# Optimization experiments

Measured on AMD Instinct MI355X. Metric: run time of the kernel, lower is better.

Reference implementation:

```python
import jax, jax.numpy as jnp
import numpy as np

EMBED_DIM = 32  # module-level constant used for the 1/sqrt(d) scale in the source
DROP_P = 0.2


def setup_inputs() -> dict:
    key = jax.random.key(0)
    kx, kq, kk, kv = jax.random.split(key, 4)
    B, T, C = 8, 4096, EMBED_DIM
    x = jax.random.normal(kx, (B, T, C), dtype=jnp.float32)
    Wq = jax.random.normal(kq, (C, C), dtype=jnp.float32) * (1.0 / np.sqrt(C))
    Wk = jax.random.normal(kk, (C, C), dtype=jnp.float32) * (1.0 / np.sqrt(C))
    Wv = jax.random.normal(kv, (C, C), dtype=jnp.float32) * (1.0 / np.sqrt(C))
    return {"x": x, "Wq": Wq, "Wk": Wk, "Wv": Wv}


def reference(x, Wq, Wk, Wv):
    B, T, C = x.shape
    # bias-free linear projections: y = x @ W.T (torch nn.Linear convention)
    q = jnp.einsum('btc,dc->btd', x, Wq)
    k = jnp.einsum('btc,dc->btd', x, Wk)
    v = jnp.einsum('btc,dc->btd', x, Wv)
    # scaled scores [B, T, T]
    att = jnp.einsum('btd,bsd->bts', q, k) / jnp.sqrt(jnp.float32(EMBED_DIM))
    causal = jnp.tril(jnp.ones((T, T), dtype=bool))
    att = jnp.where(causal, att, -jnp.inf)
    wei = jax.nn.softmax(att, axis=-1)
    # dropout on attention weights (training mode, p=0.2), deterministic key
    keep = jax.random.bernoulli(jax.random.key(42), 1.0 - DROP_P, wei.shape)
    wei = jnp.where(keep, wei / (1.0 - DROP_P), 0.0)
    return jnp.einsum('bts,bsd->btd', wei, v)
```

## Files before the change

kernel.cpp:

```cpp
#include <hip/hip_runtime.h>
#include <stdint.h>

#define BB 8
#define TTN 4096
#define CCH 32
#define WIN 128
#define KEEP_LT9 3435974144u

typedef __attribute__((ext_vector_type(8))) short bf16x8;
typedef __attribute__((ext_vector_type(4))) float f32x4;

union B8 { uint32_t u[4]; uint4 q; bf16x8 v; };

__device__ __forceinline__ uint32_t cvt_pk_bf16(float lo, float hi) {
    uint32_t d;
    asm("v_cvt_pk_bf16_f32 %0, %1, %2" : "=v"(d) : "v"(lo), "v"(hi));
    return d;
}

__device__ __forceinline__ uint32_t rotl32(uint32_t x, int r) {
    return __builtin_amdgcn_alignbit(x, x, 32 - r);
}

__device__ __forceinline__ uint32_t mask_bits(uint32_t idx) {
    uint32_t x0 = 0u, x1 = idx + 42u;
    const uint32_t K2 = 42u ^ 0x1BD11BDAu;
#define TFR(r) { x0 += x1; x1 = rotl32(x1, (r)); x1 ^= x0; }
    TFR(13) TFR(15) TFR(26) TFR(6)
    x0 += 42u; x1 += K2 + 1u;
    TFR(17) TFR(29) TFR(16) TFR(24)
    x0 += K2; x1 += 2u;
    TFR(13) TFR(15) TFR(26) TFR(6)
    x1 += 42u + 3u;
    TFR(17) TFR(29) TFR(16) TFR(24)
    x0 += 42u; x1 += K2 + 4u;
    TFR(13) TFR(15) TFR(26) TFR(6)
    x0 += K2; x1 += 5u;
#undef TFR
    return x0 ^ x1;
}

__device__ __forceinline__ void threefry4(uint32_t i0, uint32_t i1, uint32_t i2, uint32_t i3,
                                          uint32_t& o0, uint32_t& o1, uint32_t& o2, uint32_t& o3) {
    const uint32_t K2 = 42u ^ 0x1BD11BDAu;
    uint32_t a0 = 0u, a1 = 0u, a2 = 0u, a3 = 0u;
    uint32_t b0 = i0 + 42u, b1 = i1 + 42u, b2 = i2 + 42u, b3 = i3 + 42u;
#define R4(r)                                                                  \
    { a0 += b0; a1 += b1; a2 += b2; a3 += b3;                                  \
      b0 = rotl32(b0, (r)); b1 = rotl32(b1, (r));                              \
      b2 = rotl32(b2, (r)); b3 = rotl32(b3, (r));                              \
      b0 ^= a0; b1 ^= a1; b2 ^= a2; b3 ^= a3; }
#define INJ(da, db)                                                            \
    { a0 += (da); a1 += (da); a2 += (da); a3 += (da);                          \
      b0 += (db); b1 += (db); b2 += (db); b3 += (db); }
    R4(13) R4(15) R4(26) R4(6)
    INJ(42u, K2 + 1u)
    R4(17) R4(29) R4(16) R4(24)
    INJ(K2, 2u)
    R4(13) R4(15) R4(26) R4(6)
    INJ(0u, 42u + 3u)
    R4(17) R4(29) R4(16) R4(24)
    INJ(42u, K2 + 4u)
    R4(13) R4(15) R4(26) R4(6)
    INJ(K2, 5u)
#undef R4
#undef INJ
    o0 = a0 ^ b0; o1 = a1 ^ b1; o2 = a2 ^ b2; o3 = a3 ^ b3;
}

__global__ __launch_bounds__(256) void proj_qkv(const float* __restrict__ x,
                                                const float* __restrict__ Wq,
                                                const float* __restrict__ Wk,
                                                const float* __restrict__ Wv,
                                                float* __restrict__ Qf,
                                                uint16_t* __restrict__ Kb,
                                                uint16_t* __restrict__ Vt) {
    __shared__ float sW[3][CCH * CCH];
    __shared__ uint16_t vs[256][34];
    const int tid = threadIdx.x;
    for (int i = tid; i < CCH * CCH; i += 256) {
        sW[0][i] = Wq[i]; sW[1][i] = Wk[i]; sW[2][i] = Wv[i];
    }
    __syncthreads();
    const int row = blockIdx.x * 256 + tid;
    const float4* xp = reinterpret_cast<const float4*>(x + (size_t)row * CCH);
    float xr[CCH];
    #pragma unroll
    for (int i = 0; i < 8; ++i) {
        float4 t4 = xp[i];
        xr[4*i] = t4.x; xr[4*i+1] = t4.y; xr[4*i+2] = t4.z; xr[4*i+3] = t4.w;
    }
    const float scale = 0.17677669529663687f;
    #pragma unroll
    for (int mtx = 0; mtx < 3; ++mtx) {
        float o[CCH];
        #pragma unroll
        for (int d = 0; d < CCH; ++d) {
            float s0 = 0.f, s1 = 0.f, s2 = 0.f, s3 = 0.f;
            #pragma unroll
            for (int c = 0; c < CCH; c += 4) {
                s0 += xr[c]   * sW[mtx][d*CCH + c];
                s1 += xr[c+1] * sW[mtx][d*CCH + c+1];
                s2 += xr[c+2] * sW[mtx][d*CCH + c+2];
                s3 += xr[c+3] * sW[mtx][d*CCH + c+3];
            }
            o[d] = (s0 + s1) + (s2 + s3);
            if (mtx == 0) o[d] *= scale;
        }
        if (mtx == 0) {
            float4* op = reinterpret_cast<float4*>(Qf + (size_t)row * CCH);
            #pragma unroll
            for (int i = 0; i < 8; ++i)
                op[i] = make_float4(o[4*i], o[4*i+1], o[4*i+2], o[4*i+3]);
        } else if (mtx == 1) {
            uint32_t dw[16];
            #pragma unroll
            for (int k = 0; k < 16; ++k) dw[k] = cvt_pk_bf16(o[2*k], o[2*k+1]);
            uint4* kp = reinterpret_cast<uint4*>((char*)Kb + (size_t)row * 64);
            #pragma unroll
            for (int q = 0; q < 4; ++q)
                kp[q] = make_uint4(dw[4*q], dw[4*q+1], dw[4*q+2], dw[4*q+3]);
        } else {
            #pragma unroll
            for (int k = 0; k < 16; ++k)
                *reinterpret_cast<uint32_t*>(&vs[tid][2*k]) = cvt_pk_bf16(o[2*k], o[2*k+1]);
        }
    }
    __syncthreads();
    const int b = blockIdx.x >> 4, seg = blockIdx.x & 15;
    const int d = tid >> 3, part = tid & 7;
    uint32_t dw[16];
    #pragma unroll
    for (int k = 0; k < 16; ++k) {
        const uint32_t lo = vs[part*32 + 2*k][d];
        const uint32_t hi = vs[part*32 + 2*k + 1][d];
        dw[k] = lo | (hi << 16);
    }
    uint16_t* dst = Vt + (size_t)b * (CCH * TTN) + (size_t)d * TTN + seg * 256 + part * 32;
    uint4* dp = reinterpret_cast<uint4*>(dst);
    #pragma unroll
    for (int q = 0; q < 4; ++q)
        dp[q] = make_uint4(dw[4*q], dw[4*q+1], dw[4*q+2], dw[4*q+3]);
}

__global__ __launch_bounds__(512, 4) void attn_mfma(const float* __restrict__ Qf,
                                                    const uint16_t* __restrict__ Kb,
                                                    const uint16_t* __restrict__ Vt,
                                                    float* __restrict__ out) {
    __shared__ __align__(16) char smem[9728];

    const int j = blockIdx.x;
    const int b = j & 7;
    const int u = j >> 3;
    const int tile = (u < 32) ? (127 - u) : (u < 64) ? (u - 32)
                   : (u < 96) ? (159 - u) : (u - 64);

    const int w = threadIdx.x >> 6;
    const int lane = threadIdx.x & 63;
    const int tl = lane & 15;
    const int g = lane >> 4;
    const int thalf = w & 1;
    const int sg = w >> 1;
    const int slb = sg * 32;
    const int t0 = tile * 32;
    const int t_g = t0 + thalf * 16 + tl;

    const float* qrow = Qf + ((size_t)b * TTN + t_g) * CCH + g * 8;
    const float4 qa = *reinterpret_cast<const float4*>(qrow);
    const float4 qb = *reinterpret_cast<const float4*>(qrow + 4);
    B8 qf;
    qf.u[0] = cvt_pk_bf16(qa.x, qa.y); qf.u[1] = cvt_pk_bf16(qa.z, qa.w);
    qf.u[2] = cvt_pk_bf16(qb.x, qb.y); qf.u[3] = cvt_pk_bf16(qb.z, qb.w);

    f32x4 acc0 = {0.f,0.f,0.f,0.f}, acc1 = {0.f,0.f,0.f,0.f};
    float m = -1e30f, l = 0.f;

    const char* Kbb = (const char*)Kb + (size_t)b * TTN * 64;
    const char* Vbb = (const char*)Vt + (size_t)b * CCH * TTN * 2;
    const uint32_t idxb = ((uint32_t)b << 24) | ((uint32_t)t_g << 12);

    const int nwin = (32 * tile + 159) >> 7;

#define ATT_WINDOW(S0, TAIL)                                                   \
    {                                                                          \
        const int srow = (S0) + slb;                                           \
        B8 ka, kc, va, vc, pf;                                                 \
        ka.q = *reinterpret_cast<const uint4*>(Kbb + (size_t)(srow + tl) * 64 + g * 16); \
        kc.q = *reinterpret_cast<const uint4*>(Kbb + (size_t)(srow + 16 + tl) * 64 + g * 16); \
        va.q = *reinterpret_cast<const uint4*>(Vbb + (size_t)tl * 8192 + (size_t)(srow + g * 8) * 2); \
        vc.q = *reinterpret_cast<const uint4*>(Vbb + (size_t)(16 + tl) * 8192 + (size_t)(srow + g * 8) * 2); \
              \
        const uint32_t ib = idxb | (uint32_t)(srow + 4 * g);                   \
        uint32_t r0, r1, r2, r3, r4, r5, r6, r7;                               \
        threefry4(ib,       ib + 1u,  ib + 2u,  ib + 3u,  r0, r1, r2, r3);     \
        threefry4(ib + 16u, ib + 17u, ib + 18u, ib + 19u, r4, r5, r6, r7);     \
        const float f0 = (r0 < KEEP_LT9) ? 1.f : 0.f;                          \
        const float f1 = (r1 < KEEP_LT9) ? 1.f : 0.f;                          \
        const float f2 = (r2 < KEEP_LT9) ? 1.f : 0.f;                          \
        const float f3 = (r3 < KEEP_LT9) ? 1.f : 0.f;                          \
        const float f4 = (r4 < KEEP_LT9) ? 1.f : 0.f;                          \
        const float f5 = (r5 < KEEP_LT9) ? 1.f : 0.f;                          \
        const float f6 = (r6 < KEEP_LT9) ? 1.f : 0.f;                          \
        const float f7 = (r7 < KEEP_LT9) ? 1.f : 0.f;                          \
        const f32x4 zz = {0.f,0.f,0.f,0.f};                                    \
        f32x4 d0 = __builtin_amdgcn_mfma_f32_16x16x32_bf16(ka.v, qf.v, zz, 0, 0, 0); \
        f32x4 d1 = __builtin_amdgcn_mfma_f32_16x16x32_bf16(kc.v, qf.v, zz, 0, 0, 0); \
        if (TAIL) {                                                            \
            const int sv = srow + 4 * g;                                       \
            d0.x = (sv + 0  <= t_g) ? d0.x : -1e30f;                           \
            d0.y = (sv + 1  <= t_g) ? d0.y : -1e30f;                           \
            d0.z = (sv + 2  <= t_g) ? d0.z : -1e30f;                           \
            d0.w = (sv + 3  <= t_g) ? d0.w : -1e30f;                           \
            d1.x = (sv + 16 <= t_g) ? d1.x : -1e30f;                           \
            d1.y = (sv + 17 <= t_g) ? d1.y : -1e30f;                           \
            d1.z = (sv + 18 <= t_g) ? d1.z : -1e30f;                           \
            d1.w = (sv + 19 <= t_g) ? d1.w : -1e30f;                           \
        }                                                                      \
        float mx = fmaxf(fmaxf(fmaxf(d0.x, d0.y), fmaxf(d0.z, d0.w)),          \
                         fmaxf(fmaxf(d1.x, d1.y), fmaxf(d1.z, d1.w)));         \
        mx = fmaxf(mx, __shfl_xor(mx, 16));                                    \
        mx = fmaxf(mx, __shfl_xor(mx, 32));                                    \
        const bool up = mx > m + 8.0f;               \
        const float corr = up ? __expf(m - mx) : 1.0f;                         \
        m = up ? mx : m;                                                       \
        l *= corr; acc0 *= corr; acc1 *= corr;                                 \
        float p0 = __expf(d0.x - m), p1 = __expf(d0.y - m);                    \
        float p2 = __expf(d0.z - m), p3 = __expf(d0.w - m);                    \
        float p4 = __expf(d1.x - m), p5 = __expf(d1.y - m);                    \
        float p6 = __expf(d1.z - m), p7 = __expf(d1.w - m);                    \
        if (TAIL) {                                                            \
            const float alive = (srow <= t_g) ? 1.0f : 0.0f;                   \
            p0 *= alive; p1 *= alive; p2 *= alive; p3 *= alive;                \
            p4 *= alive; p5 *= alive; p6 *= alive; p7 *= alive;                \
        }                                                                      \
        float ls = ((p0 + p1) + (p2 + p3)) + ((p4 + p5) + (p6 + p7));          \
        ls += __shfl_xor(ls, 16);                                              \
        ls += __shfl_xor(ls, 32);                                              \
        l += ls;                                                               \
        const uint32_t k00 = cvt_pk_bf16(p0 * f0, p1 * f1);                    \
        const uint32_t k01 = cvt_pk_bf16(p2 * f2, p3 * f3);                    \
        const uint32_t k10 = cvt_pk_bf16(p4 * f4, p5 * f5);                    \
        const uint32_t k11 = cvt_pk_bf16(p6 * f6, p7 * f7);                    \
        const int srcA = 16 * ((g & 1) * 2) + tl;                              \
        const int srcB = srcA + 16;                                            \
        const uint32_t a0 = (uint32_t)__shfl((int)k00, srcA);                  \
        const uint32_t b0 = (uint32_t)__shfl((int)k10, srcA);                  \
        const uint32_t a1 = (uint32_t)__shfl((int)k01, srcA);                  \
        const uint32_t b1 = (uint32_t)__shfl((int)k11, srcA);                  \
        const uint32_t a2 = (uint32_t)__shfl((int)k00, srcB);                  \
        const uint32_t b2 = (uint32_t)__shfl((int)k10, srcB);                  \
        const uint32_t a3 = (uint32_t)__shfl((int)k01, srcB);                  \
        const uint32_t b3 = (uint32_t)__shfl((int)k11, srcB);                  \
        const bool hi = (g >= 2);                                              \
        pf.u[0] = hi ? b0 : a0; pf.u[1] = hi ? b1 : a1;                        \
        pf.u[2] = hi ? b2 : a2; pf.u[3] = hi ? b3 : a3;                        \
        acc0 = __builtin_amdgcn_mfma_f32_16x16x32_bf16(va.v, pf.v, acc0, 0, 0, 0); \
        acc1 = __builtin_amdgcn_mfma_f32_16x16x32_bf16(vc.v, pf.v, acc1, 0, 0, 0); \
    }

    #pragma unroll 1
    for (int win = 0; win < nwin - 1; ++win) {
        ATT_WINDOW(win << 7, 0)
    }
    {
        const int s0 = (nwin - 1) << 7;
        if (s0 + slb <= t0 + thalf * 16 + 15) ATT_WINDOW(s0, 1)
    }
#undef ATT_WINDOW

#define SLOT(TH, S) reinterpret_cast<float*>(smem + ((TH) * 2 + (S)) * 2432)
#define PUBLISH(SB)                                                            \
    {                                                                          \
        float* sb = (SB);                                                      \
        *reinterpret_cast<float4*>(sb + tl * 36 + 4 * g)      = make_float4(acc0.x, acc0.y, acc0.z, acc0.w); \
        *reinterpret_cast<float4*>(sb + tl * 36 + 16 + 4 * g) = make_float4(acc1.x, acc1.y, acc1.z, acc1.w); \
        if (g == 0) { sb[576 + 2 * tl] = m; sb[577 + 2 * tl] = l; }            \
    }
#define CONSUME(SB)                                                            \
    {                                                                          \
        const float* sb = (SB);                                                \
        const float m2 = sb[576 + 2 * tl], l2 = sb[577 + 2 * tl];              \
        const float4 x0 = *reinterpret_cast<const float4*>(sb + tl * 36 + 4 * g); \
        const float4 x1 = *reinterpret_cast<const float4*>(sb + tl * 36 + 16 + 4 * g); \
        const float mn = fmaxf(m, m2);                                         \
        const float ca = __expf(m - mn), cb = __expf(m2 - mn);                 \
        l = l * ca + l2 * cb;                                                  \
        acc0.x = acc0.x * ca + x0.x * cb; acc0.y = acc0.y * ca + x0.y * cb;    \
        acc0.z = acc0.z * ca + x0.z * cb; acc0.w = acc0.w * ca + x0.w * cb;    \
        acc1.x = acc1.x * ca + x1.x * cb; acc1.y = acc1.y * ca + x1.y * cb;    \
        acc1.z = acc1.z * ca + x1.z * cb; acc1.w = acc1.w * ca + x1.w * cb;    \
        m = mn;                                                                \
    }
    if (sg >= 2) PUBLISH(SLOT(thalf, sg - 2))
    __syncthreads();
    if (sg < 2) CONSUME(SLOT(thalf, sg))
    __syncthreads();
    if (sg == 1) PUBLISH(SLOT(thalf, 0))
    __syncthreads();
    if (sg == 0) {
        CONSUME(SLOT(thalf, 0))
        const float inv = 1.0f / (0.8f * l);
        float* orow = out + ((size_t)b * TTN + t_g) * CCH;
        *reinterpret_cast<float4*>(orow + 4 * g) =
            make_float4(acc0.x * inv, acc0.y * inv, acc0.z * inv, acc0.w * inv);
        *reinterpret_cast<float4*>(orow + 16 + 4 * g) =
            make_float4(acc1.x * inv, acc1.y * inv, acc1.z * inv, acc1.w * inv);
    }
#undef SLOT
#undef PUBLISH
#undef CONSUME
}

extern "C" void kernel_launch(void* const* d_in, const int* in_sizes, int n_in,
                              void* d_out, int out_size, void* d_ws, size_t ws_size,
                              hipStream_t stream) {
    const float* x  = (const float*)d_in[0];
    const float* Wq = (const float*)d_in[1];
    const float* Wk = (const float*)d_in[2];
    const float* Wv = (const float*)d_in[3];
    float* outp = (float*)d_out;

    float*    Qf = (float*)d_ws;
    uint16_t* Kb = (uint16_t*)((char*)d_ws + 4194304);
    uint16_t* Vt = (uint16_t*)((char*)d_ws + 6291456);

    proj_qkv<<<(BB * TTN) / 256, 256, 0, stream>>>(x, Wq, Wk, Wv, Qf, Kb, Vt);
    attn_mfma<<<1024, 512, 0, stream>>>(Qf, Kb, Vt, outp);
}
```

Baseline: 168.2 us.

## Split attention blocks into 16-row halves with 256 threads and longest-first ordering

Each attention block now handles one 16-query half-tile with 4 waves instead of both halves with 8 waves, doubling the grid to 2048 blocks of 256 threads. Tiles are issued in strictly descending causal length instead of the previous interleaved order, and the loop count is computed per half so the shorter half skips unneeded windows. The dropout mask is also applied as a select on the probability rather than a multiply by a 0/1 factor. The intent is finer-grained load balancing and less wasted work on causal tails, at the cost of loading K/V separately for each half.

```diff
diff --git a/kernel.cpp b/kernel.cpp
--- a/kernel.cpp
+++ b/kernel.cpp
@@ -20,24 +20,6 @@
 
 __device__ __forceinline__ uint32_t rotl32(uint32_t x, int r) {
     return __builtin_amdgcn_alignbit(x, x, 32 - r);
-}
-
-__device__ __forceinline__ uint32_t mask_bits(uint32_t idx) {
-    uint32_t x0 = 0u, x1 = idx + 42u;
-    const uint32_t K2 = 42u ^ 0x1BD11BDAu;
-#define TFR(r) { x0 += x1; x1 = rotl32(x1, (r)); x1 ^= x0; }
-    TFR(13) TFR(15) TFR(26) TFR(6)
-    x0 += 42u; x1 += K2 + 1u;
-    TFR(17) TFR(29) TFR(16) TFR(24)
-    x0 += K2; x1 += 2u;
-    TFR(13) TFR(15) TFR(26) TFR(6)
-    x1 += 42u + 3u;
-    TFR(17) TFR(29) TFR(16) TFR(24)
-    x0 += 42u; x1 += K2 + 4u;
-    TFR(13) TFR(15) TFR(26) TFR(6)
-    x0 += K2; x1 += 5u;
-#undef TFR
-    return x0 ^ x1;
 }
 
 __device__ __forceinline__ void threefry4(uint32_t i0, uint32_t i1, uint32_t i2, uint32_t i3,
@@ -143,27 +125,25 @@
         dp[q] = make_uint4(dw[4*q], dw[4*q+1], dw[4*q+2], dw[4*q+3]);
 }
 
-__global__ __launch_bounds__(512, 4) void attn_mfma(const float* __restrict__ Qf,
+__global__ __launch_bounds__(256, 8) void attn_mfma(const float* __restrict__ Qf,
                                                     const uint16_t* __restrict__ Kb,
                                                     const uint16_t* __restrict__ Vt,
                                                     float* __restrict__ out) {
-    __shared__ __align__(16) char smem[9728];
+    __shared__ __align__(16) char smem[4864];
 
     const int j = blockIdx.x;
     const int b = j & 7;
-    const int u = j >> 3;
-    const int tile = (u < 32) ? (127 - u) : (u < 64) ? (u - 32)
-                   : (u < 96) ? (159 - u) : (u - 64);
+    const int thalf = (j >> 3) & 1;
+    const int tile = 127 - (j >> 4);
 
     const int w = threadIdx.x >> 6;
     const int lane = threadIdx.x & 63;
     const int tl = lane & 15;
     const int g = lane >> 4;
-    const int thalf = w & 1;
-    const int sg = w >> 1;
+    const int sg = w;
     const int slb = sg * 32;
-    const int t0 = tile * 32;
-    const int t_g = t0 + thalf * 16 + tl;
+    const int tbase = tile * 32 + thalf * 16;
+    const int t_g = tbase + tl;
 
     const float* qrow = Qf + ((size_t)b * TTN + t_g) * CCH + g * 8;
     const float4 qa = *reinterpret_cast<const float4*>(qrow);
@@ -179,7 +159,7 @@
     const char* Vbb = (const char*)Vt + (size_t)b * CCH * TTN * 2;
     const uint32_t idxb = ((uint32_t)b << 24) | ((uint32_t)t_g << 12);
 
-    const int nwin = (32 * tile + 159) >> 7;
+    const int nwin = ((tbase + 15) >> 7) + 1;
 
 #define ATT_WINDOW(S0, TAIL)                                                   \
     {                                                                          \
@@ -189,19 +169,11 @@
         kc.q = *reinterpret_cast<const uint4*>(Kbb + (size_t)(srow + 16 + tl) * 64 + g * 16); \
         va.q = *reinterpret_cast<const uint4*>(Vbb + (size_t)tl * 8192 + (size_t)(srow + g * 8) * 2); \
         vc.q = *reinterpret_cast<const uint4*>(Vbb + (size_t)(16 + tl) * 8192 + (size_t)(srow + g * 8) * 2); \
-              \
+               \
         const uint32_t ib = idxb | (uint32_t)(srow + 4 * g);                   \
         uint32_t r0, r1, r2, r3, r4, r5, r6, r7;                               \
         threefry4(ib,       ib + 1u,  ib + 2u,  ib + 3u,  r0, r1, r2, r3);     \
         threefry4(ib + 16u, ib + 17u, ib + 18u, ib + 19u, r4, r5, r6, r7);     \
-        const float f0 = (r0 < KEEP_LT9) ? 1.f : 0.f;                          \
-        const float f1 = (r1 < KEEP_LT9) ? 1.f : 0.f;                          \
-        const float f2 = (r2 < KEEP_LT9) ? 1.f : 0.f;                          \
-        const float f3 = (r3 < KEEP_LT9) ? 1.f : 0.f;                          \
-        const float f4 = (r4 < KEEP_LT9) ? 1.f : 0.f;                          \
-        const float f5 = (r5 < KEEP_LT9) ? 1.f : 0.f;                          \
-        const float f6 = (r6 < KEEP_LT9) ? 1.f : 0.f;                          \
-        const float f7 = (r7 < KEEP_LT9) ? 1.f : 0.f;                          \
         const f32x4 zz = {0.f,0.f,0.f,0.f};                                    \
         f32x4 d0 = __builtin_amdgcn_mfma_f32_16x16x32_bf16(ka.v, qf.v, zz, 0, 0, 0); \
         f32x4 d1 = __builtin_amdgcn_mfma_f32_16x16x32_bf16(kc.v, qf.v, zz, 0, 0, 0); \
@@ -237,10 +209,16 @@
         ls += __shfl_xor(ls, 16);                                              \
         ls += __shfl_xor(ls, 32);                                              \
         l += ls;                                                               \
-        const uint32_t k00 = cvt_pk_bf16(p0 * f0, p1 * f1);                    \
-        const uint32_t k01 = cvt_pk_bf16(p2 * f2, p3 * f3);                    \
-        const uint32_t k10 = cvt_pk_bf16(p4 * f4, p5 * f5);                    \
-        const uint32_t k11 = cvt_pk_bf16(p6 * f6, p7 * f7);                    \
+        const float q0 = (r0 < KEEP_LT9) ? p0 : 0.f;        \
+        const float q1 = (r1 < KEEP_LT9) ? p1 : 0.f;                           \
+        const float q2 = (r2 < KEEP_LT9) ? p2 : 0.f;                           \
+        const float q3 = (r3 < KEEP_LT9) ? p3 : 0.f;                           \
+        const float q4 = (r4 < KEEP_LT9) ? p4 : 0.f;                           \
+        const float q5 = (r5 < KEEP_LT9) ? p5 : 0.f;                           \
+        const float q6 = (r6 < KEEP_LT9) ? p6 : 0.f;                           \
+        const float q7 = (r7 < KEEP_LT9) ? p7 : 0.f;                           \
+        const uint32_t k00 = cvt_pk_bf16(q0, q1), k01 = cvt_pk_bf16(q2, q3);   \
+        const uint32_t k10 = cvt_pk_bf16(q4, q5), k11 = cvt_pk_bf16(q6, q7);   \
         const int srcA = 16 * ((g & 1) * 2) + tl;                              \
         const int srcB = srcA + 16;                                            \
         const uint32_t a0 = (uint32_t)__shfl((int)k00, srcA);                  \
@@ -264,11 +242,11 @@
     }
     {
         const int s0 = (nwin - 1) << 7;
-        if (s0 + slb <= t0 + thalf * 16 + 15) ATT_WINDOW(s0, 1)
+        if (s0 + slb <= tbase + 15) ATT_WINDOW(s0, 1)
     }
 #undef ATT_WINDOW
 
-#define SLOT(TH, S) reinterpret_cast<float*>(smem + ((TH) * 2 + (S)) * 2432)
+#define SLOT(S) reinterpret_cast<float*>(smem + (S) * 2432)
 #define PUBLISH(SB)                                                            \
     {                                                                          \
         float* sb = (SB);                                                      \
@@ -291,14 +269,14 @@
         acc1.z = acc1.z * ca + x1.z * cb; acc1.w = acc1.w * ca + x1.w * cb;    \
         m = mn;                                                                \
     }
-    if (sg >= 2) PUBLISH(SLOT(thalf, sg - 2))
-    __syncthreads();
-    if (sg < 2) CONSUME(SLOT(thalf, sg))
-    __syncthreads();
-    if (sg == 1) PUBLISH(SLOT(thalf, 0))
+    if (sg >= 2) PUBLISH(SLOT(sg - 2))
+    __syncthreads();
+    if (sg < 2) CONSUME(SLOT(sg))
+    __syncthreads();
+    if (sg == 1) PUBLISH(SLOT(0))
     __syncthreads();
     if (sg == 0) {
-        CONSUME(SLOT(thalf, 0))
+        CONSUME(SLOT(0))
         const float inv = 1.0f / (0.8f * l);
         float* orow = out + ((size_t)b * TTN + t_g) * CCH;
         *reinterpret_cast<float4*>(orow + 4 * g) =
@@ -325,5 +303,5 @@
     uint16_t* Vt = (uint16_t*)((char*)d_ws + 6291456);
 
     proj_qkv<<<(BB * TTN) / 256, 256, 0, stream>>>(x, Wq, Wk, Wv, Qf, Kb, Vt);
-    attn_mfma<<<1024, 512, 0, stream>>>(Qf, Kb, Vt, outp);
-}
+    attn_mfma<<<2048, 256, 0, stream>>>(Qf, Kb, Vt, outp);
+}
```

After: 171.1 us. No clear change (+1.7%).
